# Performance work log

Hardware: AMD Instinct MI355X
Metric: run time of the kernel (lower is better)

Reference implementation:

```python
import jax, jax.numpy as jnp
import numpy as np


def setup_inputs() -> dict:
    key = jax.random.key(0)
    k1, k2 = jax.random.split(key)
    batch, d_model, L = 4096, 1024, 2048
    # binary inputs in {0,1} as in torch.randint(0, 2, ...)
    x = jax.random.randint(k1, (batch, L), 0, 2, dtype=jnp.int32)
    references = jax.random.randint(k2, (d_model, L), 0, 2).astype(jnp.float32)
    return {"x": x, "references": references}


def reference(x, references):
    # Hamming distance between binary vectors a,b in {0,1}:
    #   sum(a != b) = sum(a) + sum(b) - 2 * a.b
    # This avoids materializing the (batch, d_model, L) broadcast tensor
    # while computing exactly the same values as the original module.
    L = x.shape[-1]
    xf = x.astype(jnp.float32)                     # (B, L)
    dot = jnp.einsum('bl,dl->bd', xf, references)  # (B, D)
    sum_x = jnp.sum(xf, axis=-1, keepdims=True)    # (B, 1)
    sum_r = jnp.sum(references, axis=-1)           # (D,)
    hamming = sum_x + sum_r[None, :] - 2.0 * dot   # (B, D)
    mean = L / 2
    std = 0.5 * (L ** 0.5)
    return (hamming - mean) / std
```

## Files before the change

### kernel.cpp

```cpp
#include <hip/hip_runtime.h>
#include <stdint.h>

constexpr int B_ROWS = 4096;
constexpr int D_ROWS = 1024;
constexpr int L_LEN  = 2048;
constexpr int LB     = L_LEN / 2;

using int32x4 = __attribute__((ext_vector_type(4))) int;
using int32x8 = __attribute__((ext_vector_type(8))) int;
using f32x16  = __attribute__((ext_vector_type(16))) float;

constexpr int XSEGS = B_ROWS * 4;
constexpr int RSEGS = D_ROWS * 4;
constexpr int CVT_BLOCKS = (XSEGS + RSEGS) / 4;

__global__ __launch_bounds__(256) void convert_fp4_kernel(
    const int* __restrict__ x, const float* __restrict__ r,
    uint32_t* __restrict__ xq, uint32_t* __restrict__ rq)
{
  const int wave = (int)((blockIdx.x * blockDim.x + threadIdx.x) >> 6);
  const int lane = threadIdx.x & 63;
  uint32_t wo;
  if (wave < XSEGS) {
    const int row = wave >> 2, seg = wave & 3;
    const int* s = x + (size_t)row * L_LEN + seg * 512 + lane * 4;
    const int4 v0 = *reinterpret_cast<const int4*>(s);
    const int4 v1 = *reinterpret_cast<const int4*>(s + 256);
    wo  = (v0.x ? 0xAu : 0x2u);
    wo |= (v0.y ? 0xAu : 0x2u) << 4;
    wo |= (v0.z ? 0xAu : 0x2u) << 8;
    wo |= (v0.w ? 0xAu : 0x2u) << 12;
    wo |= (v1.x ? 0xAu : 0x2u) << 16;
    wo |= (v1.y ? 0xAu : 0x2u) << 20;
    wo |= (v1.z ? 0xAu : 0x2u) << 24;
    wo |= (v1.w ? 0xAu : 0x2u) << 28;
    xq[row * 256 + seg * 64 + lane] = wo;
  } else {
    const int sr  = wave - XSEGS;
    const int row = sr >> 2, seg = sr & 3;
    const float* s = r + (size_t)row * L_LEN + seg * 512 + lane * 4;
    const float4 v0 = *reinterpret_cast<const float4*>(s);
    const float4 v1 = *reinterpret_cast<const float4*>(s + 256);
    wo  = (v0.x != 0.0f ? 0xAu : 0x2u);
    wo |= (v0.y != 0.0f ? 0xAu : 0x2u) << 4;
    wo |= (v0.z != 0.0f ? 0xAu : 0x2u) << 8;
    wo |= (v0.w != 0.0f ? 0xAu : 0x2u) << 12;
    wo |= (v1.x != 0.0f ? 0xAu : 0x2u) << 16;
    wo |= (v1.y != 0.0f ? 0xAu : 0x2u) << 20;
    wo |= (v1.z != 0.0f ? 0xAu : 0x2u) << 24;
    wo |= (v1.w != 0.0f ? 0xAu : 0x2u) << 28;
    rq[row * 256 + seg * 64 + lane] = wo;
  }
}

constexpr int BM = 128;
constexpr int BN = 64;
constexpr int BKB = 64;
constexpr int KSTEPS = LB / BKB;
constexpr int GRID_D = D_ROWS / BN;
constexpr int NWG = (B_ROWS / BM) * GRID_D;

typedef __attribute__((address_space(3))) void       as3_void;
typedef const __attribute__((address_space(1))) void as1_cvoid;

__device__ __forceinline__ void gload_lds16(const void* g, void* l) {
  __builtin_amdgcn_global_load_lds((as1_cvoid*)g, (as3_void*)l, 16, 0, 0);
}

__global__ __launch_bounds__(256) void gemm_fp4_kernel(
    const uint8_t* __restrict__ Aq, const uint8_t* __restrict__ Bq,
    float* __restrict__ out)
{
  __shared__ __align__(16) uint8_t A_lds[3][BM * BKB];
  __shared__ __align__(16) uint8_t B_lds[3][BN * BKB];

  const int lin = blockIdx.x;
  const int swz = (lin & 7) * (NWG / 8) + (lin >> 3);
  const int bm  = (swz / GRID_D) * BM;
  const int bn  = (swz % GRID_D) * BN;

  const int t    = threadIdx.x;
  const int lane = t & 63;
  const int w    = t >> 6;
  const int wr   = w >> 1;
  const int wc   = w & 1;

  const uint8_t* gA[2];
#pragma unroll
  for (int c = 0; c < 2; ++c) {
    const int r = w * 32 + c * 16 + (lane >> 2);
    gA[c] = Aq + (size_t)(bm + r) * LB + (((lane & 3) ^ ((r >> 1) & 3)) * 16);
  }
  const int rB = w * 16 + (lane >> 2);
  const uint8_t* gB0 =
      Bq + (size_t)(bn + rB) * LB + (((lane & 3) ^ ((rB >> 1) & 3)) * 16);

#define STAGE(buf, k0b) do {                                                  \
    _Pragma("unroll") for (int _c = 0; _c < 2; ++_c)                          \
      gload_lds16(gA[_c] + (k0b), A_lds[buf] + (w * 32 + _c * 16) * BKB);     \
    gload_lds16(gB0 + (k0b), B_lds[buf] + (w * 16) * BKB);                    \
  } while (0)

#define COMPUTE(cur) do {                                                     \
    _Pragma("unroll") for (int kc = 0; kc < 2; ++kc) {                        \
      const int rowB = wc * 32 + (lane & 31);                                 \
      const int qB   = 2 * kc + (lane >> 5);                                  \
      const int32x4 b4 = *reinterpret_cast<const int32x4*>(                   \
          B_lds[cur] + rowB * BKB + ((qB ^ ((rowB >> 1) & 3)) * 16));         \
      const int32x8 b8 = {b4[0], b4[1], b4[2], b4[3], 0, 0, 0, 0};            \
      _Pragma("unroll") for (int f = 0; f < 2; ++f) {                         \
        const int rowA = wr * 64 + f * 32 + (lane & 31);                      \
        const int qA   = 2 * kc + (lane >> 5);                                \
        const int32x4 a4 = *reinterpret_cast<const int32x4*>(                 \
            A_lds[cur] + rowA * BKB + ((qA ^ ((rowA >> 1) & 3)) * 16));       \
        const int32x8 a8 = {a4[0], a4[1], a4[2], a4[3], 0, 0, 0, 0};          \
        acc[f] = __builtin_amdgcn_mfma_scale_f32_32x32x64_f8f6f4(             \
            a8, b8, acc[f], 4, 4, 0, 0x7F7F7F7F, 0, 0x7F7F7F7F);              \
      }                                                                       \
    } } while (0)

  f32x16 acc[2] = {};

  STAGE(0, 0);
  STAGE(1, BKB);

#pragma unroll 3
  for (int ks = 0; ks < KSTEPS - 1; ++ks) {
    const int cur = ks % 3;
    asm volatile("s_waitcnt vmcnt(3)" ::: "memory");
    __builtin_amdgcn_sched_barrier(0);
    __builtin_amdgcn_s_barrier();
    if (ks + 2 < KSTEPS) STAGE((ks + 2) % 3, (ks + 2) * BKB);
    COMPUTE(cur);
  }
  asm volatile("s_waitcnt vmcnt(0)" ::: "memory");
  __builtin_amdgcn_sched_barrier(0);
  __builtin_amdgcn_s_barrier();
  COMPUTE(0);

#undef STAGE
#undef COMPUTE

  const float scale = -0.5f * 0.04419417382415922f;
  const int col = bn + wc * 32 + (lane & 31);
#pragma unroll
  for (int f = 0; f < 2; ++f) {
#pragma unroll
    for (int reg = 0; reg < 16; ++reg) {
      const int row = bm + wr * 64 + f * 32 + (reg & 3) + 8 * (reg >> 2)
                    + 4 * (lane >> 5);
      out[(size_t)row * D_ROWS + col] = acc[f][reg] * scale;
    }
  }
}

extern "C" void kernel_launch(void* const* d_in, const int* in_sizes, int n_in,
                              void* d_out, int out_size, void* d_ws, size_t ws_size,
                              hipStream_t stream) {
  const int*   x = (const int*)d_in[0];
  const float* r = (const float*)d_in[1];
  float*     out = (float*)d_out;

  uint8_t* Aq = (uint8_t*)d_ws;
  uint8_t* Bq = Aq + (size_t)B_ROWS * LB;

  convert_fp4_kernel<<<CVT_BLOCKS, 256, 0, stream>>>(
      x, r, (uint32_t*)Aq, (uint32_t*)Bq);

  gemm_fp4_kernel<<<NWG, 256, 0, stream>>>(Aq, Bq, out);
}
```

Baseline: 25.00 us.

## Fuse FP4 conversion and GEMM into one cooperative kernel with grid sync

```diff
diff --git a/kernel.cpp b/kernel.cpp
--- a/kernel.cpp
+++ b/kernel.cpp
@@ -1,5 +1,8 @@
 #include <hip/hip_runtime.h>
+#include <hip/hip_cooperative_groups.h>
 #include <stdint.h>
+
+namespace cg = cooperative_groups;
 
 constexpr int B_ROWS = 4096;
 constexpr int D_ROWS = 1024;
@@ -10,55 +13,16 @@
 using int32x8 = __attribute__((ext_vector_type(8))) int;
 using f32x16  = __attribute__((ext_vector_type(16))) float;
 
-constexpr int XSEGS = B_ROWS * 4;
-constexpr int RSEGS = D_ROWS * 4;
-constexpr int CVT_BLOCKS = (XSEGS + RSEGS) / 4;
-
-__global__ __launch_bounds__(256) void convert_fp4_kernel(
-    const int* __restrict__ x, const float* __restrict__ r,
-    uint32_t* __restrict__ xq, uint32_t* __restrict__ rq)
-{
-  const int wave = (int)((blockIdx.x * blockDim.x + threadIdx.x) >> 6);
-  const int lane = threadIdx.x & 63;
-  uint32_t wo;
-  if (wave < XSEGS) {
-    const int row = wave >> 2, seg = wave & 3;
-    const int* s = x + (size_t)row * L_LEN + seg * 512 + lane * 4;
-    const int4 v0 = *reinterpret_cast<const int4*>(s);
-    const int4 v1 = *reinterpret_cast<const int4*>(s + 256);
-    wo  = (v0.x ? 0xAu : 0x2u);
-    wo |= (v0.y ? 0xAu : 0x2u) << 4;
-    wo |= (v0.z ? 0xAu : 0x2u) << 8;
-    wo |= (v0.w ? 0xAu : 0x2u) << 12;
-    wo |= (v1.x ? 0xAu : 0x2u) << 16;
-    wo |= (v1.y ? 0xAu : 0x2u) << 20;
-    wo |= (v1.z ? 0xAu : 0x2u) << 24;
-    wo |= (v1.w ? 0xAu : 0x2u) << 28;
-    xq[row * 256 + seg * 64 + lane] = wo;
-  } else {
-    const int sr  = wave - XSEGS;
-    const int row = sr >> 2, seg = sr & 3;
-    const float* s = r + (size_t)row * L_LEN + seg * 512 + lane * 4;
-    const float4 v0 = *reinterpret_cast<const float4*>(s);
-    const float4 v1 = *reinterpret_cast<const float4*>(s + 256);
-    wo  = (v0.x != 0.0f ? 0xAu : 0x2u);
-    wo |= (v0.y != 0.0f ? 0xAu : 0x2u) << 4;
-    wo |= (v0.z != 0.0f ? 0xAu : 0x2u) << 8;
-    wo |= (v0.w != 0.0f ? 0xAu : 0x2u) << 12;
-    wo |= (v1.x != 0.0f ? 0xAu : 0x2u) << 16;
-    wo |= (v1.y != 0.0f ? 0xAu : 0x2u) << 20;
-    wo |= (v1.z != 0.0f ? 0xAu : 0x2u) << 24;
-    wo |= (v1.w != 0.0f ? 0xAu : 0x2u) << 28;
-    rq[row * 256 + seg * 64 + lane] = wo;
-  }
-}
-
 constexpr int BM = 128;
 constexpr int BN = 64;
 constexpr int BKB = 64;
 constexpr int KSTEPS = LB / BKB;
 constexpr int GRID_D = D_ROWS / BN;
 constexpr int NWG = (B_ROWS / BM) * GRID_D;
+constexpr int NWAVES = NWG * 4;
+
+constexpr int XSEGS = B_ROWS * 4;
+constexpr int RSEGS = D_ROWS * 4;
 
 typedef __attribute__((address_space(3))) void       as3_void;
 typedef const __attribute__((address_space(1))) void as1_cvoid;
@@ -67,12 +31,56 @@
   __builtin_amdgcn_global_load_lds((as1_cvoid*)g, (as3_void*)l, 16, 0, 0);
 }
 
-__global__ __launch_bounds__(256) void gemm_fp4_kernel(
-    const uint8_t* __restrict__ Aq, const uint8_t* __restrict__ Bq,
+__global__ __launch_bounds__(256) void fused_kernel(
+    const int* __restrict__ x, const float* __restrict__ r,
+    uint8_t* __restrict__ Aq, uint8_t* __restrict__ Bq,
     float* __restrict__ out)
 {
   __shared__ __align__(16) uint8_t A_lds[3][BM * BKB];
   __shared__ __align__(16) uint8_t B_lds[3][BN * BKB];
+
+  const int lane = threadIdx.x & 63;
+
+  {
+    uint32_t* xq = (uint32_t*)Aq;
+    uint32_t* rq = (uint32_t*)Bq;
+    const int gwave = (int)((blockIdx.x * blockDim.x + threadIdx.x) >> 6);
+    for (int sgi = gwave; sgi < XSEGS + RSEGS; sgi += NWAVES) {
+      uint32_t wo;
+      if (sgi < XSEGS) {
+        const int row = sgi >> 2, seg = sgi & 3;
+        const int* s = x + (size_t)row * L_LEN + seg * 512 + lane * 4;
+        const int4 v0 = *reinterpret_cast<const int4*>(s);
+        const int4 v1 = *reinterpret_cast<const int4*>(s + 256);
+        wo  = (v0.x ? 0xAu : 0x2u);
+        wo |= (v0.y ? 0xAu : 0x2u) << 4;
+        wo |= (v0.z ? 0xAu : 0x2u) << 8;
+        wo |= (v0.w ? 0xAu : 0x2u) << 12;
+        wo |= (v1.x ? 0xAu : 0x2u) << 16;
+        wo |= (v1.y ? 0xAu : 0x2u) << 20;
+        wo |= (v1.z ? 0xAu : 0x2u) << 24;
+        wo |= (v1.w ? 0xAu : 0x2u) << 28;
+        xq[row * 256 + seg * 64 + lane] = wo;
+      } else {
+        const int sr  = sgi - XSEGS;
+        const int row = sr >> 2, seg = sr & 3;
+        const float* s = r + (size_t)row * L_LEN + seg * 512 + lane * 4;
+        const float4 v0 = *reinterpret_cast<const float4*>(s);
+        const float4 v1 = *reinterpret_cast<const float4*>(s + 256);
+        wo  = (v0.x != 0.0f ? 0xAu : 0x2u);
+        wo |= (v0.y != 0.0f ? 0xAu : 0x2u) << 4;
+        wo |= (v0.z != 0.0f ? 0xAu : 0x2u) << 8;
+        wo |= (v0.w != 0.0f ? 0xAu : 0x2u) << 12;
+        wo |= (v1.x != 0.0f ? 0xAu : 0x2u) << 16;
+        wo |= (v1.y != 0.0f ? 0xAu : 0x2u) << 20;
+        wo |= (v1.z != 0.0f ? 0xAu : 0x2u) << 24;
+        wo |= (v1.w != 0.0f ? 0xAu : 0x2u) << 28;
+        rq[row * 256 + seg * 64 + lane] = wo;
+      }
+    }
+  }
+
+  cg::this_grid().sync();
 
   const int lin = blockIdx.x;
   const int swz = (lin & 7) * (NWG / 8) + (lin >> 3);
@@ -80,7 +88,6 @@
   const int bn  = (swz % GRID_D) * BN;
 
   const int t    = threadIdx.x;
-  const int lane = t & 63;
   const int w    = t >> 6;
   const int wr   = w >> 1;
   const int wc   = w & 1;
@@ -88,8 +95,8 @@
   const uint8_t* gA[2];
 #pragma unroll
   for (int c = 0; c < 2; ++c) {
-    const int r = w * 32 + c * 16 + (lane >> 2);
-    gA[c] = Aq + (size_t)(bm + r) * LB + (((lane & 3) ^ ((r >> 1) & 3)) * 16);
+    const int rr = w * 32 + c * 16 + (lane >> 2);
+    gA[c] = Aq + (size_t)(bm + rr) * LB + (((lane & 3) ^ ((rr >> 1) & 3)) * 16);
   }
   const int rB = w * 16 + (lane >> 2);
   const uint8_t* gB0 =
@@ -164,8 +171,7 @@
   uint8_t* Aq = (uint8_t*)d_ws;
   uint8_t* Bq = Aq + (size_t)B_ROWS * LB;
 
-  convert_fp4_kernel<<<CVT_BLOCKS, 256, 0, stream>>>(
-      x, r, (uint32_t*)Aq, (uint32_t*)Bq);
-
-  gemm_fp4_kernel<<<NWG, 256, 0, stream>>>(Aq, Bq, out);
+  void* kargs[] = {(void*)&x, (void*)&r, (void*)&Aq, (void*)&Bq, (void*)&out};
+  hipLaunchCooperativeKernel((const void*)fused_kernel, dim3(NWG), dim3(256),
+                             kargs, 0, stream);
 }
```

Measured after the change: 81.51 us. 226% more time.
